# Kernel optimization log

Measured on AMD Instinct MI355X. Metric: run time of the kernel, lower is better.

## Reference

```python
import jax, jax.numpy as jnp
import numpy as np

B, S, K_DIM = 2, 2048, 2048
H, H_KV = 32, 8
HD = K_DIM // H  # 64
THETA = 10000.0


def apply_rope(x, position_ids, theta):
    # x: (B, H, S, hd), position_ids: (B, S) -- interleaved (even/odd) RoPE
    hd = x.shape[-1]
    dtype = x.dtype
    inv_freq = 1.0 / theta ** (jnp.arange(0, hd, 2, dtype=dtype) / hd)  # (hd/2,)
    freqs = position_ids.astype(dtype)[:, :, None] * inv_freq           # (B, S, hd/2)
    sin = jnp.sin(freqs)[:, None]  # (B, 1, S, hd/2)
    cos = jnp.cos(freqs)[:, None]
    x1 = x[..., ::2]
    x2 = x[..., 1::2]
    even = x1 * cos - x2 * sin
    odd = x2 * cos + x1 * sin
    return jnp.stack([even, odd], axis=-1).reshape(x.shape)


def setup_inputs() -> dict:
    key = jax.random.key(0)
    ks = jax.random.split(key, 5)
    x = jax.random.normal(ks[0], (B, S, K_DIM), dtype=jnp.float32)
    position_ids = jnp.broadcast_to(jnp.arange(S, dtype=jnp.int32)[None, :], (B, S))
    attention_mask = jnp.ones((B, S), dtype=jnp.int32)
    scale = 0.02
    Wq = jax.random.normal(ks[1], (H * HD, K_DIM), dtype=jnp.float32) * scale
    Wk = jax.random.normal(ks[2], (H_KV * HD, K_DIM), dtype=jnp.float32) * scale
    Wv = jax.random.normal(ks[3], (H_KV * HD, K_DIM), dtype=jnp.float32) * scale
    Wo = jax.random.normal(ks[4], (K_DIM, K_DIM), dtype=jnp.float32) * scale
    return {"x": x, "position_ids": position_ids, "attention_mask": attention_mask,
            "Wq": Wq, "Wk": Wk, "Wv": Wv, "Wo": Wo}


def reference(x, position_ids, attention_mask, Wq, Wk, Wv, Wo):
    b, s, kd = x.shape
    hd = HD
    q = (x @ Wq.T).reshape(b, s, H, hd).transpose(0, 2, 1, 3)     # (B, H, S, hd)
    k = (x @ Wk.T).reshape(b, s, H_KV, hd).transpose(0, 2, 1, 3)  # (B, Hkv, S, hd)
    v = (x @ Wv.T).reshape(b, s, H_KV, hd).transpose(0, 2, 1, 3)
    q = apply_rope(q, position_ids, THETA)
    k = apply_rope(k, position_ids, THETA)
    rep = H // H_KV
    # repeat_interleave over head dim == expand-within-group then flatten
    k = jnp.broadcast_to(k[:, :, None], (b, H_KV, rep, s, hd)).reshape(b, H, s, hd)
    v = jnp.broadcast_to(v[:, :, None], (b, H_KV, rep, s, hd)).reshape(b, H, s, hd)
    causal = jnp.triu(jnp.ones((s, s), dtype=bool), 1)            # True = masked
    pad = (attention_mask == 0)[:, None, None, :]                 # (B,1,1,S)
    mask = causal[None, None, :, :] | pad                         # (B,1,S,S) -> broadcast over H
    scores = jnp.einsum('bhqd,bhkd->bhqk', q, k) / jnp.sqrt(jnp.asarray(hd, x.dtype))
    scores = jnp.where(mask, jnp.finfo(scores.dtype).min, scores)
    attn = jax.nn.softmax(scores, axis=-1)
    out = jnp.einsum('bhqk,bhkd->bhqd', attn, v)
    out = out.transpose(0, 2, 1, 3).reshape(b, s, kd)
    return out @ Wo.T
```

## Files before the change

### kernel.cpp

```cpp
#include <hip/hip_runtime.h>
#include <hip/hip_bf16.h>

#define S_LEN 2048
#define BATCH 2
#define KDIM  2048
#define NH    32
#define NKV   8
#define HDIM  64

typedef short bf16s;
typedef short bf16x8 __attribute__((ext_vector_type(8)));
typedef short bf16x4 __attribute__((ext_vector_type(4)));
typedef float f32x4  __attribute__((ext_vector_type(4)));

#define KSCALE 0.1803368801111f

__device__ __forceinline__ bf16s f2bf(float f) {
  __hip_bfloat16 h = __float2bfloat16(f);
  return *reinterpret_cast<bf16s*>(&h);
}
__device__ __forceinline__ float ex2(float x) { return __builtin_amdgcn_exp2f(x); }

__device__ __forceinline__ void gload16(const void* g, void* l) {
  __builtin_amdgcn_global_load_lds(
      (const __attribute__((address_space(1))) char*)g,
      (__attribute__((address_space(3))) char*)l, 16, 0, 0);
}

__global__ void k_cvt_all(const float* __restrict__ s0, const float* __restrict__ s1,
                          const float* __restrict__ s2, const float* __restrict__ s3,
                          const float* __restrict__ s4, bf16s* __restrict__ dst,
                          float* __restrict__ qtab, float* __restrict__ ktab,
                          const int* __restrict__ pos) {
  const int t = blockIdx.x * blockDim.x + threadIdx.x;
  if (t < S_LEN * 32) {
    const int p = t >> 5, i = t & 31;
    const float inv = expf(-(float)(2 * i) * (1.0f / 64.0f) * 9.210340371976184f);
    const float fr = (float)p * inv;
    const float c = cosf(fr), s = sinf(fr);
    ktab[2 * t]     = c;
    ktab[2 * t + 1] = s;
    qtab[2 * t]     = c * KSCALE;
    qtab[2 * t + 1] = s * KSCALE;
  }
  const int NU = 2359296;
  const int stride = gridDim.x * blockDim.x;
  for (int u = t; u < NU; u += stride) {
    const int e = u * 8;
    const float* src; int off;
    if (e < 8388608)       { src = s0; off = e; }
    else if (e < 12582912) { src = s1; off = e - 8388608; }
    else if (e < 13631488) { src = s2; off = e - 12582912; }
    else if (e < 14680064) { src = s3; off = e - 13631488; }
    else                   { src = s4; off = e - 14680064; }
    float4 a = *(const float4*)(src + off);
    float4 b = *(const float4*)(src + off + 4);
    bf16x8 o;
    o[0]=f2bf(a.x); o[1]=f2bf(a.y); o[2]=f2bf(a.z); o[3]=f2bf(a.w);
    o[4]=f2bf(b.x); o[5]=f2bf(b.y); o[6]=f2bf(b.z); o[7]=f2bf(b.w);
    *(bf16x8*)(dst + e) = o;
  }
}

__global__ __launch_bounds__(256, 2)
void k_gemm_qkv(const bf16s* __restrict__ A, const bf16s* __restrict__ Bw,
                const int* __restrict__ pos,
                const float* __restrict__ qtab, const float* __restrict__ ktab,
                bf16s* __restrict__ qb, bf16s* __restrict__ kb, bf16s* __restrict__ vtb) {
  const int K = KDIM;
  __shared__ bf16s As[128 * 32];
  __shared__ bf16s Bs[128 * 32];
  const int tid  = threadIdx.x;
  const int lane = tid & 63;
  const int w    = tid >> 6;
  const int wr   = w >> 1, wc = w & 1;
  const int l15  = lane & 15, lg = lane >> 4;
  const int h0 = blockIdx.y * 24 + blockIdx.x;
  const int sw = (h0 & 7) * 96 + (h0 >> 3);
  const int bx = sw % 24;
  const int by = sw / 24;

  f32x4 acc[4][4] = {};

  const bf16s* gA0 = A  + (size_t)(by * 128 + (tid >> 2)) * K + ((tid & 3) << 3);
  const bf16s* gA1 = gA0 + (size_t)64 * K;
  const bf16s* gB0 = Bw + (size_t)(bx * 128 + (tid >> 2)) * K + ((tid & 3) << 3);
  const bf16s* gB1 = gB0 + (size_t)64 * K;
  bf16s* lA0 = &As[w * 512];
  bf16s* lA1 = &As[2048 + w * 512];
  bf16s* lB0 = &Bs[w * 512];
  bf16s* lB1 = &Bs[2048 + w * 512];

  const int nkt = K >> 5;
  for (int kt = 0; kt < nkt; ++kt) {
    __syncthreads();
    const int ko = kt << 5;
    gload16(gA0 + ko, lA0);
    gload16(gA1 + ko, lA1);
    gload16(gB0 + ko, lB0);
    gload16(gB1 + ko, lB1);
    __syncthreads();

    const bf16s* pa = &As[(wr * 64 + l15) * 32 + lg * 8];
    const bf16s* pb = &Bs[(wc * 64 + l15) * 32 + lg * 8];
    bf16x8 av[4], bv[4];
#pragma unroll
    for (int i = 0; i < 4; ++i) {
      av[i] = *(const bf16x8*)(pa + i * 512);
      bv[i] = *(const bf16x8*)(pb + i * 512);
    }
#pragma unroll
    for (int mi = 0; mi < 4; ++mi)
#pragma unroll
      for (int ni = 0; ni < 4; ++ni)
        acc[mi][ni] = __builtin_amdgcn_mfma_f32_16x16x32_bf16(av[mi], bv[ni], acc[mi][ni], 0, 0, 0);
  }

#pragma unroll
  for (int mi = 0; mi < 4; ++mi) {
    const int m0 = by * 128 + wr * 64 + mi * 16 + 4 * lg;
#pragma unroll
    for (int ni = 0; ni < 4; ++ni) {
      const int n = bx * 128 + wc * 64 + ni * 16 + l15;
      if (bx < 16) {
        const int d = n & 63, i = d >> 1;
        const float sgn = (d & 1) ? 1.f : -1.f;
#pragma unroll
        for (int r = 0; r < 4; ++r) {
          const int m = m0 + r;
          const float val = acc[mi][ni][r];
          const float par = __shfl_xor(val, 1);
          const float2 cs = *(const float2*)&qtab[((size_t)pos[m] << 6) + (i << 1)];
          qb[(size_t)m * KDIM + n] = f2bf(val * cs.x + sgn * par * cs.y);
        }
      } else if (bx < 20) {
        const int col = n - 2048;
        const int d = col & 63, i = d >> 1;
        const float sgn = (d & 1) ? 1.f : -1.f;
#pragma unroll
        for (int r = 0; r < 4; ++r) {
          const int m = m0 + r;
          const float val = acc[mi][ni][r];
          const float par = __shfl_xor(val, 1);
          const float2 cs = *(const float2*)&ktab[((size_t)pos[m] << 6) + (i << 1)];
          kb[(size_t)m * 512 + col] = f2bf(val * cs.x + sgn * par * cs.y);
        }
      } else {
        const int col = n - 2560;
        const int kvh = col >> 6, d = col & 63;
        const int b = m0 >> 11, s = m0 & (S_LEN - 1);
        bf16x4 pk;
#pragma unroll
        for (int r = 0; r < 4; ++r) pk[r] = f2bf(acc[mi][ni][r]);
        *(bf16x4*)&vtb[((size_t)((b * NKV + kvh) * HDIM + d)) * S_LEN + s] = pk;
      }
    }
  }
}

__global__ __launch_bounds__(256, 2)
void k_gemm_o(const bf16s* __restrict__ A, const bf16s* __restrict__ Bw,
              float* __restrict__ C, int N, int K) {
  __shared__ bf16s As[128 * 32];
  __shared__ bf16s Bs[128 * 32];
  const int tid  = threadIdx.x;
  const int lane = tid & 63;
  const int w    = tid >> 6;
  const int wr   = w >> 1, wc = w & 1;
  const int l15  = lane & 15, lg = lane >> 4;
  const int h0 = blockIdx.y * 16 + blockIdx.x;
  const int sw = (h0 & 7) * 64 + (h0 >> 3);
  const int bx = sw & 15;
  const int by = sw >> 4;

  f32x4 acc[4][4] = {};

  const bf16s* gA0 = A  + (size_t)(by * 128 + (tid >> 2)) * K + ((tid & 3) << 3);
  const bf16s* gA1 = gA0 + (size_t)64 * K;
  const bf16s* gB0 = Bw + (size_t)(bx * 128 + (tid >> 2)) * K + ((tid & 3) << 3);
  const bf16s* gB1 = gB0 + (size_t)64 * K;
  bf16s* lA0 = &As[w * 512];
  bf16s* lA1 = &As[2048 + w * 512];
  bf16s* lB0 = &Bs[w * 512];
  bf16s* lB1 = &Bs[2048 + w * 512];

  const int nkt = K >> 5;
  for (int kt = 0; kt < nkt; ++kt) {
    __syncthreads();
    const int ko = kt << 5;
    gload16(gA0 + ko, lA0);
    gload16(gA1 + ko, lA1);
    gload16(gB0 + ko, lB0);
    gload16(gB1 + ko, lB1);
    __syncthreads();

    const bf16s* pa = &As[(wr * 64 + l15) * 32 + lg * 8];
    const bf16s* pb = &Bs[(wc * 64 + l15) * 32 + lg * 8];
    bf16x8 av[4], bv[4];
#pragma unroll
    for (int i = 0; i < 4; ++i) {
      av[i] = *(const bf16x8*)(pa + i * 512);
      bv[i] = *(const bf16x8*)(pb + i * 512);
    }
#pragma unroll
    for (int mi = 0; mi < 4; ++mi)
#pragma unroll
      for (int ni = 0; ni < 4; ++ni)
        acc[mi][ni] = __builtin_amdgcn_mfma_f32_16x16x32_bf16(av[mi], bv[ni], acc[mi][ni], 0, 0, 0);
  }

#pragma unroll
  for (int mi = 0; mi < 4; ++mi) {
    const int m0 = by * 128 + wr * 64 + mi * 16 + 4 * lg;
#pragma unroll
    for (int ni = 0; ni < 4; ++ni) {
      const int n = bx * 128 + wc * 64 + ni * 16 + l15;
#pragma unroll
      for (int r = 0; r < 4; ++r)
        C[(size_t)(m0 + r) * N + n] = acc[mi][ni][r];
    }
  }
}

__global__ __launch_bounds__(256, 3)
void k_flash(const bf16s* __restrict__ q, const bf16s* __restrict__ k,
             const bf16s* __restrict__ vt, const int* __restrict__ amask,
             bf16s* __restrict__ out) {
  __shared__ bf16s Ks[2][64 * 64];
  __shared__ bf16s Vs[2][64 * 64];
  __shared__ bf16s Ps[4][32 * 64];

  const int tid = threadIdx.x, lane = tid & 63, w = tid >> 6;
  const int l15 = lane & 15, lg = lane >> 4;
  const int bh = blockIdx.x;
  const int y = blockIdx.y, yq = y & 3, hi = (y >> 3) & 1;
  const int qt = (y & 4) ? (yq + (hi << 2)) : ((hi ? 11 : 15) - yq);
  const int b = bh >> 5, h = bh & 31, kvh = h >> 2;
  const int nt = 2 * qt + 2;

  bf16x8 aq[2][2];
  const int qbase = qt * 128 + w * 32;
#pragma unroll
  for (int u = 0; u < 2; ++u) {
    const size_t qr = (size_t)(b * S_LEN + qbase + u * 16 + l15);
#pragma unroll
    for (int s = 0; s < 2; ++s)
      aq[u][s] = *(const bf16x8*)(q + qr * KDIM + h * HDIM + s * 32 + lg * 8);
  }

  const bf16s* kbase = k + (size_t)b * S_LEN * (NKV * HDIM) + kvh * HDIM;
  const bf16s* vbase = vt + ((size_t)(b * NKV + kvh) * HDIM) * S_LEN;

  const int srow0 = w * 16 + (lane >> 3);
  const int scol0 = (lane & 7) ^ (srow0 & 7);
  const int srow1 = srow0 + 8;
  const int scol1 = (lane & 7) ^ (srow1 & 7);

  auto stage = [&](int kt, int bufi) {
    gload16(kbase + (size_t)(kt * 64 + srow0) * (NKV * HDIM) + scol0 * 8, &Ks[bufi][w * 1024]);
    gload16(kbase + (size_t)(kt * 64 + srow1) * (NKV * HDIM) + scol1 * 8, &Ks[bufi][w * 1024 + 512]);
    gload16(vbase + (size_t)srow0 * S_LEN + kt * 64 + scol0 * 8, &Vs[bufi][w * 1024]);
    gload16(vbase + (size_t)srow1 * S_LEN + kt * 64 + scol1 * 8, &Vs[bufi][w * 1024 + 512]);
  };

  float m_run[2] = {-1e30f, -1e30f}, l_run[2] = {0.f, 0.f};
  f32x4 ao[2][4] = {};

  stage(0, 0);
  __syncthreads();

  int buf = 0;
  for (int kt = 0; kt < nt; ++kt) {
    if (kt + 1 < nt) stage(kt + 1, buf ^ 1);

    const unsigned long long bm = __ballot(amask[b * S_LEN + kt * 64 + lane] != 0);
    const bool allok = (bm == ~0ull);
    const bool diag = (kt >= nt - 2);

    f32x4 sc[2][4] = {};
    __builtin_amdgcn_s_setprio(1);
#pragma unroll
    for (int c = 0; c < 4; ++c) {
      const int row = c * 16 + l15;
      const bf16s* kp = &Ks[buf][row * 64];
      const int xw = (row & 7) << 3;
      bf16x8 kb0 = *(const bf16x8*)(kp + ((lg * 8) ^ xw));
      bf16x8 kb1 = *(const bf16x8*)(kp + ((32 + lg * 8) ^ xw));
      sc[0][c] = __builtin_amdgcn_mfma_f32_16x16x32_bf16(kb0, aq[0][0], sc[0][c], 0, 0, 0);
      sc[0][c] = __builtin_amdgcn_mfma_f32_16x16x32_bf16(kb1, aq[0][1], sc[0][c], 0, 0, 0);
      sc[1][c] = __builtin_amdgcn_mfma_f32_16x16x32_bf16(kb0, aq[1][0], sc[1][c], 0, 0, 0);
      sc[1][c] = __builtin_amdgcn_mfma_f32_16x16x32_bf16(kb1, aq[1][1], sc[1][c], 0, 0, 0);
    }
    __builtin_amdgcn_s_setprio(0);

#pragma unroll
    for (int u = 0; u < 2; ++u) {
      const int qg = qt * 128 + w * 32 + u * 16 + l15;
      float mt = -1e30f;
      if (diag || !allok) {
#pragma unroll
        for (int c = 0; c < 4; ++c)
#pragma unroll
          for (int r = 0; r < 4; ++r) {
            const int kg = kt * 64 + c * 16 + lg * 4 + r;
            float s = sc[u][c][r];
            if ((kg > qg) || (!allok && !((bm >> (kg & 63)) & 1))) s = -1e30f;
            sc[u][c][r] = s;
            mt = fmaxf(mt, s);
          }
      } else {
#pragma unroll
        for (int c = 0; c < 4; ++c)
#pragma unroll
          for (int r = 0; r < 4; ++r) mt = fmaxf(mt, sc[u][c][r]);
      }
      mt = fmaxf(mt, __shfl_xor(mt, 16));
      mt = fmaxf(mt, __shfl_xor(mt, 32));
      if (!__all(mt <= m_run[u])) {
        const float mn = fmaxf(m_run[u], mt);
        const float al = ex2(m_run[u] - mn);
        m_run[u] = mn;
        l_run[u] *= al;
#pragma unroll
        for (int vc = 0; vc < 4; ++vc)
#pragma unroll
          for (int r = 0; r < 4; ++r) ao[u][vc][r] *= al;
      }
      const float mb = m_run[u];
      float ls = 0.f;
#pragma unroll
      for (int c = 0; c < 4; ++c) {
        bf16x4 pk;
#pragma unroll
        for (int r = 0; r < 4; ++r) {
          const float p = ex2(sc[u][c][r] - mb);
          ls += p;
          pk[r] = f2bf(p);
        }
        const int prow = u * 16 + l15;
        *(bf16x4*)&Ps[w][prow * 64 + ((c * 16 + lg * 4) ^ ((prow & 7) << 3))] = pk;
      }
      ls += __shfl_xor(ls, 16);
      ls += __shfl_xor(ls, 32);
      l_run[u] += ls;
    }

    bf16x8 pa[2][2];
#pragma unroll
    for (int u = 0; u < 2; ++u) {
      const int prow = u * 16 + l15;
      const int px = (prow & 7) << 3;
#pragma unroll
      for (int s = 0; s < 2; ++s)
        pa[u][s] = *(const bf16x8*)&Ps[w][prow * 64 + ((s * 32 + lg * 8) ^ px)];
    }

    __builtin_amdgcn_s_setprio(1);
#pragma unroll
    for (int vc = 0; vc < 4; ++vc) {
      const int row = vc * 16 + l15;
      const bf16s* vp = &Vs[buf][row * 64];
      const int xw = (row & 7) << 3;
      bf16x8 vb0 = *(const bf16x8*)(vp + ((lg * 8) ^ xw));
      bf16x8 vb1 = *(const bf16x8*)(vp + ((32 + lg * 8) ^ xw));
      ao[0][vc] = __builtin_amdgcn_mfma_f32_16x16x32_bf16(vb0, pa[0][0], ao[0][vc], 0, 0, 0);
      ao[0][vc] = __builtin_amdgcn_mfma_f32_16x16x32_bf16(vb1, pa[0][1], ao[0][vc], 0, 0, 0);
      ao[1][vc] = __builtin_amdgcn_mfma_f32_16x16x32_bf16(vb0, pa[1][0], ao[1][vc], 0, 0, 0);
      ao[1][vc] = __builtin_amdgcn_mfma_f32_16x16x32_bf16(vb1, pa[1][1], ao[1][vc], 0, 0, 0);
    }
    __builtin_amdgcn_s_setprio(0);

    __syncthreads();
    buf ^= 1;
  }

#pragma unroll
  for (int u = 0; u < 2; ++u) {
    const float inv = 1.0f / l_run[u];
    const size_t m = (size_t)b * S_LEN + qt * 128 + w * 32 + u * 16 + l15;
#pragma unroll
    for (int vc = 0; vc < 4; ++vc) {
      bf16x4 ov;
#pragma unroll
      for (int r = 0; r < 4; ++r) ov[r] = f2bf(ao[u][vc][r] * inv);
      *(bf16x4*)&out[m * KDIM + h * HDIM + vc * 16 + lg * 4] = ov;
    }
  }
}

extern "C" void kernel_launch(void* const* d_in, const int* in_sizes, int n_in,
                              void* d_out, int out_size, void* d_ws, size_t ws_size,
                              hipStream_t stream) {
  const float* x  = (const float*)d_in[0];
  const int* pos  = (const int*)d_in[1];
  const int* am   = (const int*)d_in[2];
  const float* Wq = (const float*)d_in[3];
  const float* Wk = (const float*)d_in[4];
  const float* Wv = (const float*)d_in[5];
  const float* Wo = (const float*)d_in[6];
  float* out = (float*)d_out;

  char* ws = (char*)d_ws;
  const int M = BATCH * S_LEN;
  bf16s* xb   = (bf16s*)(ws);
  bf16s* wqkv = (bf16s*)(ws + 16777216);
  bf16s* wob  = (bf16s*)(ws + 29360128);
  bf16s* qb   = (bf16s*)(ws + 37748736);
  bf16s* kb   = (bf16s*)(ws + 54525952);
  bf16s* vtb  = (bf16s*)(ws + 58720256);
  bf16s* aob  = (bf16s*)(ws + 62914560);
  float* qtab = (float*)(ws + 62914560);
  float* ktab = (float*)(ws + 63438848);

  dim3 blk(256);

  k_cvt_all<<<dim3(2048), blk, 0, stream>>>(x, Wq, Wk, Wv, Wo, xb, qtab, ktab, pos);

  k_gemm_qkv<<<dim3(24, 32), blk, 0, stream>>>(xb, wqkv, pos, qtab, ktab, qb, kb, vtb);

  k_flash<<<dim3(BATCH * NH, S_LEN / 128), blk, 0, stream>>>(qb, kb, vtb, am, aob);

  k_gemm_o<<<dim3(16, 32), blk, 0, stream>>>(aob, wob, out, 2048, 2048);
}
```

Before: 195.5 us.

## Double GEMM K-tile to 64 with XOR-swizzled LDS layout

Both projection GEMM kernels now stage a 64-wide K slice per iteration instead of 32, which halves the number of barrier pairs per output tile. The shared-memory rows are stored with an XOR swizzle on 16-byte chunks, applied on both the global-to-LDS load and the fragment reads, to avoid LDS bank conflicts. LDS use per block doubles to 32 KB, which may limit occupancy, though two blocks per CU should still fit.

```diff
diff --git a/kernel.cpp b/kernel.cpp
--- a/kernel.cpp
+++ b/kernel.cpp
@@ -68,8 +68,8 @@
                 const float* __restrict__ qtab, const float* __restrict__ ktab,
                 bf16s* __restrict__ qb, bf16s* __restrict__ kb, bf16s* __restrict__ vtb) {
   const int K = KDIM;
-  __shared__ bf16s As[128 * 32];
-  __shared__ bf16s Bs[128 * 32];
+  __shared__ bf16s As[128 * 64];
+  __shared__ bf16s Bs[128 * 64];
   const int tid  = threadIdx.x;
   const int lane = tid & 63;
   const int w    = tid >> 6;
@@ -82,38 +82,40 @@
 
   f32x4 acc[4][4] = {};
 
-  const bf16s* gA0 = A  + (size_t)(by * 128 + (tid >> 2)) * K + ((tid & 3) << 3);
-  const bf16s* gA1 = gA0 + (size_t)64 * K;
-  const bf16s* gB0 = Bw + (size_t)(bx * 128 + (tid >> 2)) * K + ((tid & 3) << 3);
-  const bf16s* gB1 = gB0 + (size_t)64 * K;
-  bf16s* lA0 = &As[w * 512];
-  bf16s* lA1 = &As[2048 + w * 512];
-  bf16s* lB0 = &Bs[w * 512];
-  bf16s* lB1 = &Bs[2048 + w * 512];
-
-  const int nkt = K >> 5;
+  const int srow = (w << 3) + (lane >> 3);
+  const int sc8  = ((lane & 7) ^ (lane >> 3)) << 3;
+  const bf16s* gA = A  + (size_t)(by * 128 + srow) * K + sc8;
+  const bf16s* gB = Bw + (size_t)(bx * 128 + srow) * K + sc8;
+  bf16s* lA = &As[(w << 3) * 64];
+  bf16s* lB = &Bs[(w << 3) * 64];
+
+  const int nkt = K >> 6;
   for (int kt = 0; kt < nkt; ++kt) {
     __syncthreads();
-    const int ko = kt << 5;
-    gload16(gA0 + ko, lA0);
-    gload16(gA1 + ko, lA1);
-    gload16(gB0 + ko, lB0);
-    gload16(gB1 + ko, lB1);
+    const int ko = kt << 6;
+#pragma unroll
+    for (int j = 0; j < 4; ++j) {
+      gload16(gA + (size_t)(j * 32) * K + ko, lA + j * 2048);
+      gload16(gB + (size_t)(j * 32) * K + ko, lB + j * 2048);
+    }
     __syncthreads();
 
-    const bf16s* pa = &As[(wr * 64 + l15) * 32 + lg * 8];
-    const bf16s* pb = &Bs[(wc * 64 + l15) * 32 + lg * 8];
-    bf16x8 av[4], bv[4];
-#pragma unroll
-    for (int i = 0; i < 4; ++i) {
-      av[i] = *(const bf16x8*)(pa + i * 512);
-      bv[i] = *(const bf16x8*)(pb + i * 512);
-    }
-#pragma unroll
-    for (int mi = 0; mi < 4; ++mi)
-#pragma unroll
-      for (int ni = 0; ni < 4; ++ni)
-        acc[mi][ni] = __builtin_amdgcn_mfma_f32_16x16x32_bf16(av[mi], bv[ni], acc[mi][ni], 0, 0, 0);
+#pragma unroll
+    for (int kk = 0; kk < 2; ++kk) {
+      bf16x8 av[4], bv[4];
+#pragma unroll
+      for (int i = 0; i < 4; ++i) {
+        const int ra = wr * 64 + i * 16 + l15;
+        av[i] = *(const bf16x8*)&As[ra * 64 + ((kk * 32 + lg * 8) ^ ((ra & 7) << 3))];
+        const int rb = wc * 64 + i * 16 + l15;
+        bv[i] = *(const bf16x8*)&Bs[rb * 64 + ((kk * 32 + lg * 8) ^ ((rb & 7) << 3))];
+      }
+#pragma unroll
+      for (int mi = 0; mi < 4; ++mi)
+#pragma unroll
+        for (int ni = 0; ni < 4; ++ni)
+          acc[mi][ni] = __builtin_amdgcn_mfma_f32_16x16x32_bf16(av[mi], bv[ni], acc[mi][ni], 0, 0, 0);
+    }
   }
 
 #pragma unroll
@@ -161,8 +163,8 @@
 __global__ __launch_bounds__(256, 2)
 void k_gemm_o(const bf16s* __restrict__ A, const bf16s* __restrict__ Bw,
               float* __restrict__ C, int N, int K) {
-  __shared__ bf16s As[128 * 32];
-  __shared__ bf16s Bs[128 * 32];
+  __shared__ bf16s As[128 * 64];
+  __shared__ bf16s Bs[128 * 64];
   const int tid  = threadIdx.x;
   const int lane = tid & 63;
   const int w    = tid >> 6;
@@ -175,38 +177,40 @@
 
   f32x4 acc[4][4] = {};
 
-  const bf16s* gA0 = A  + (size_t)(by * 128 + (tid >> 2)) * K + ((tid & 3) << 3);
-  const bf16s* gA1 = gA0 + (size_t)64 * K;
-  const bf16s* gB0 = Bw + (size_t)(bx * 128 + (tid >> 2)) * K + ((tid & 3) << 3);
-  const bf16s* gB1 = gB0 + (size_t)64 * K;
-  bf16s* lA0 = &As[w * 512];
-  bf16s* lA1 = &As[2048 + w * 512];
-  bf16s* lB0 = &Bs[w * 512];
-  bf16s* lB1 = &Bs[2048 + w * 512];
-
-  const int nkt = K >> 5;
+  const int srow = (w << 3) + (lane >> 3);
+  const int sc8  = ((lane & 7) ^ (lane >> 3)) << 3;
+  const bf16s* gA = A  + (size_t)(by * 128 + srow) * K + sc8;
+  const bf16s* gB = Bw + (size_t)(bx * 128 + srow) * K + sc8;
+  bf16s* lA = &As[(w << 3) * 64];
+  bf16s* lB = &Bs[(w << 3) * 64];
+
+  const int nkt = K >> 6;
   for (int kt = 0; kt < nkt; ++kt) {
     __syncthreads();
-    const int ko = kt << 5;
-    gload16(gA0 + ko, lA0);
-    gload16(gA1 + ko, lA1);
-    gload16(gB0 + ko, lB0);
-    gload16(gB1 + ko, lB1);
+    const int ko = kt << 6;
+#pragma unroll
+    for (int j = 0; j < 4; ++j) {
+      gload16(gA + (size_t)(j * 32) * K + ko, lA + j * 2048);
+      gload16(gB + (size_t)(j * 32) * K + ko, lB + j * 2048);
+    }
     __syncthreads();
 
-    const bf16s* pa = &As[(wr * 64 + l15) * 32 + lg * 8];
-    const bf16s* pb = &Bs[(wc * 64 + l15) * 32 + lg * 8];
-    bf16x8 av[4], bv[4];
-#pragma unroll
-    for (int i = 0; i < 4; ++i) {
-      av[i] = *(const bf16x8*)(pa + i * 512);
-      bv[i] = *(const bf16x8*)(pb + i * 512);
-    }
-#pragma unroll
-    for (int mi = 0; mi < 4; ++mi)
-#pragma unroll
-      for (int ni = 0; ni < 4; ++ni)
-        acc[mi][ni] = __builtin_amdgcn_mfma_f32_16x16x32_bf16(av[mi], bv[ni], acc[mi][ni], 0, 0, 0);
+#pragma unroll
+    for (int kk = 0; kk < 2; ++kk) {
+      bf16x8 av[4], bv[4];
+#pragma unroll
+      for (int i = 0; i < 4; ++i) {
+        const int ra = wr * 64 + i * 16 + l15;
+        av[i] = *(const bf16x8*)&As[ra * 64 + ((kk * 32 + lg * 8) ^ ((ra & 7) << 3))];
+        const int rb = wc * 64 + i * 16 + l15;
+        bv[i] = *(const bf16x8*)&Bs[rb * 64 + ((kk * 32 + lg * 8) ^ ((rb & 7) << 3))];
+      }
+#pragma unroll
+      for (int mi = 0; mi < 4; ++mi)
+#pragma unroll
+        for (int ni = 0; ni < 4; ++ni)
+          acc[mi][ni] = __builtin_amdgcn_mfma_f32_16x16x32_bf16(av[mi], bv[ni], acc[mi][ni], 0, 0, 0);
+    }
   }
 
 #pragma unroll
```

Result: faster. 187.9 us (median of 4 runs) (-3.9%).
